# Optimization experiments

Measured on AMD Instinct MI355X. Metric: run time of the kernel, lower is better.

Reference implementation:

```python
import jax, jax.numpy as jnp
import numpy as np

B, N = 128, 196
ENC, DEC, ATT = 2048, 512, 512

def setup_inputs() -> dict:
    key = jax.random.key(0)
    ks = jax.random.split(key, 8)
    s_enc = 1.0 / np.sqrt(ENC)
    s_dec = 1.0 / np.sqrt(DEC)
    s_att = 1.0 / np.sqrt(ATT)
    return {
        "encoder_out": jax.random.normal(ks[0], (B, N, ENC), jnp.float32),
        "decoder_hidden": jax.random.normal(ks[1], (B, DEC), jnp.float32),
        "W_enc": jax.random.uniform(ks[2], (ENC, ATT), jnp.float32, -s_enc, s_enc),
        "b_enc": jax.random.uniform(ks[3], (ATT,), jnp.float32, -s_enc, s_enc),
        "W_dec": jax.random.uniform(ks[4], (DEC, ATT), jnp.float32, -s_dec, s_dec),
        "b_dec": jax.random.uniform(ks[5], (ATT,), jnp.float32, -s_dec, s_dec),
        "W_full": jax.random.uniform(ks[6], (ATT,), jnp.float32, -s_att, s_att),
        "b_full": jax.random.uniform(ks[7], (), jnp.float32, -s_att, s_att),
    }

def reference(encoder_out, decoder_hidden, W_enc, b_enc, W_dec, b_dec, W_full, b_full):
    # att1: [B, N, ATT]; att2: [B, 1, ATT]
    att1 = jnp.einsum('bne,ea->bna', encoder_out, W_enc) + b_enc
    att2 = decoder_hidden @ W_dec + b_dec
    combined = jax.nn.relu(att1 + att2[:, None, :])
    e = jnp.einsum('bna,a->bn', combined, W_full) + b_full  # [B, N]
    alpha = jax.nn.softmax(e, axis=1)
    attention_weighted_encoding = jnp.einsum('bne,bn->be', encoder_out, alpha)
    return attention_weighted_encoding, alpha
```

## Files before the change

kernel.cpp:

```cpp
#include <hip/hip_runtime.h>
#include <hip/hip_bf16.h>

#define BB   128
#define NN   196
#define MM   (BB*NN)
#define ENC  2048
#define ATT  512
#define DEC  512
#define BK   32
#define KSTEPS (ENC/BK)

using f32x4 = __attribute__((ext_vector_type(4))) float;
using s16x8 = __attribute__((ext_vector_type(8))) short;
using u16x4 = __attribute__((ext_vector_type(4))) unsigned short;
using u16x8 = __attribute__((ext_vector_type(8))) unsigned short;

__device__ __forceinline__ short f2bf(float f) {
    union { __hip_bfloat16 h; short s; } u;
    u.h = __float2bfloat16(f);
    return u.s;
}
__device__ __forceinline__ float bf2f(unsigned short u) {
    union { unsigned int i; float f; } v;
    v.i = ((unsigned int)u) << 16;
    return v.f;
}

__global__ void transpose_convert_kernel(const float* __restrict__ W,
                                         unsigned short* __restrict__ Wt) {
    __shared__ float tile[32][33];
    const int a0 = blockIdx.x * 32;
    const int k0 = blockIdx.y * 32;
    const int tx = threadIdx.x & 31, ty = threadIdx.x >> 5;
    #pragma unroll
    for (int i = 0; i < 32; i += 8)
        tile[ty + i][tx] = W[(size_t)(k0 + ty + i) * ATT + a0 + tx];
    __syncthreads();
    #pragma unroll
    for (int i = 0; i < 32; i += 8) {
        union { __hip_bfloat16 h; unsigned short u; } v;
        v.h = __float2bfloat16(tile[tx][ty + i]);
        Wt[(size_t)(a0 + ty + i) * ENC + k0 + tx] = v.u;
    }
}

__global__ __launch_bounds__(256)
void enc_cvt_kernel(const float* __restrict__ enc,
                    unsigned short* __restrict__ encb) {
    const size_t row = blockIdx.x;
    const int t = threadIdx.x;
    const float* in = enc + row * ENC + t * 8;
    f32x4 a = *(const f32x4*)in;
    f32x4 b = *(const f32x4*)(in + 4);
    u16x8 o;
    #pragma unroll
    for (int j = 0; j < 4; ++j) {
        o[j]     = (unsigned short)f2bf(a[j]);
        o[4 + j] = (unsigned short)f2bf(b[j]);
    }
    *(u16x8*)(encb + row * ENC + t * 8) = o;
}

__global__ void att2_kernel(const float* __restrict__ dec,
                            const float* __restrict__ Wd,
                            const float* __restrict__ bd,
                            const float* __restrict__ benc,
                            float* __restrict__ att2) {
    const int b  = blockIdx.x;
    const int c0 = blockIdx.y * 64;
    const int t  = threadIdx.x;
    const int cl = t & 63, kg = t >> 6;
    __shared__ float sdec[DEC];
    __shared__ float red[4][64];
    sdec[t]       = dec[b * DEC + t];
    sdec[t + 256] = dec[b * DEC + t + 256];
    __syncthreads();
    float acc = 0.f;
    const float* wp = Wd + c0 + cl;
    #pragma unroll 8
    for (int k = kg * 128; k < kg * 128 + 128; ++k)
        acc += sdec[k] * wp[(size_t)k * ATT];
    red[kg][cl] = acc;
    __syncthreads();
    if (t < 64) {
        float s = red[0][t] + red[1][t] + red[2][t] + red[3][t];
        att2[b * ATT + c0 + t] = s + bd[c0 + t] + benc[c0 + t];
    }
}

__global__ __launch_bounds__(256, 4)
void gemm_bf16_kernel(const unsigned short* __restrict__ encb,
                      const unsigned short* __restrict__ Wt,
                      const float* __restrict__ att2,
                      const float* __restrict__ Wf,
                      float* __restrict__ e_part) {
    __shared__ unsigned short sA[64 * 32];
    __shared__ unsigned short sB[256 * 32];
    __shared__ float e_sm[64];

    const int t    = threadIdx.x;
    const int lane = t & 63;
    const int w    = t >> 6;
    const int aBlk  = blockIdx.x;
    const int mBase = blockIdx.y * 64;
    const int aBase = aBlk * 256;
    const int r = lane & 15, q = lane >> 4;

    const unsigned short* gA = encb + (size_t)(mBase + (t >> 2)) * ENC + (t & 3) * 8;
    const unsigned short* gB[4];
    #pragma unroll
    for (int i = 0; i < 4; ++i) {
        int s = i * 256 + t;
        gB[i] = Wt + (size_t)(aBase + (s >> 2)) * ENC + (s & 3) * 8;
    }

    int offA[4];
    #pragma unroll
    for (int mi = 0; mi < 4; ++mi)
        offA[mi] = (mi * 16 + r) * 64 + q * 16;
    int offB[4];
    #pragma unroll
    for (int ni = 0; ni < 4; ++ni)
        offB[ni] = (w * 64 + ni * 16 + r) * 64 + q * 16;

    f32x4 acc[4][4] = {};

    #pragma unroll 1
    for (int ks = 0; ks < KSTEPS; ++ks) {
        __builtin_amdgcn_global_load_lds(
            (const __attribute__((address_space(1))) void*)(gA + (size_t)ks * BK),
            (__attribute__((address_space(3))) void*)((char*)sA + t * 16),
            16, 0, 0);
        #pragma unroll
        for (int i = 0; i < 4; ++i)
            __builtin_amdgcn_global_load_lds(
                (const __attribute__((address_space(1))) void*)(gB[i] + (size_t)ks * BK),
                (__attribute__((address_space(3))) void*)((char*)sB + (i * 256 + t) * 16),
                16, 0, 0);
        __syncthreads();

        s16x8 af[4], bf[4];
        #pragma unroll
        for (int mi = 0; mi < 4; ++mi)
            af[mi] = *(const s16x8*)((const char*)sA + offA[mi]);
        #pragma unroll
        for (int ni = 0; ni < 4; ++ni)
            bf[ni] = *(const s16x8*)((const char*)sB + offB[ni]);

        #pragma unroll
        for (int mi = 0; mi < 4; ++mi)
            #pragma unroll
            for (int ni = 0; ni < 4; ++ni)
                acc[mi][ni] = __builtin_amdgcn_mfma_f32_16x16x32_bf16(
                    af[mi], bf[ni], acc[mi][ni], 0, 0, 0);
        __syncthreads();
    }

    if (t < 64) e_sm[t] = 0.f;
    __syncthreads();

    float wfv[4];
    #pragma unroll
    for (int ni = 0; ni < 4; ++ni)
        wfv[ni] = Wf[aBase + w * 64 + ni * 16 + r];

    #pragma unroll
    for (int mi = 0; mi < 4; ++mi) {
        #pragma unroll
        for (int reg = 0; reg < 4; ++reg) {
            int lrow = mi * 16 + q * 4 + reg;
            int gm = mBase + lrow;
            int b = gm / NN;
            const float* a2 = att2 + b * ATT + aBase + w * 64;
            float rs = 0.f;
            #pragma unroll
            for (int ni = 0; ni < 4; ++ni) {
                float v = acc[mi][ni][reg] + a2[ni * 16 + r];
                rs += fmaxf(v, 0.f) * wfv[ni];
            }
            rs += __shfl_xor(rs, 1);
            rs += __shfl_xor(rs, 2);
            rs += __shfl_xor(rs, 4);
            rs += __shfl_xor(rs, 8);
            if (r == 0) atomicAdd(&e_sm[lrow], rs);
        }
    }
    __syncthreads();
    if (t < 64)
        e_part[(size_t)aBlk * MM + mBase + t] = e_sm[t];
}

__global__ __launch_bounds__(256, 5)
void gemm_e_kernel(const float* __restrict__ enc,
                   const unsigned short* __restrict__ Wt,
                   const float* __restrict__ att2,
                   const float* __restrict__ Wf,
                   float* __restrict__ e_part) {
    __shared__ float sA[64 * 32];
    __shared__ unsigned short sB[128 * 32];
    __shared__ float e_sm[64];

    const int t    = threadIdx.x;
    const int lane = t & 63;
    const int w    = t >> 6;
    const int aBlk  = blockIdx.x;
    const int mBase = blockIdx.y * 64;
    const int aBase = aBlk * 128;
    const int r = lane & 15, q = lane >> 4;

    const float* gA[2];
    #pragma unroll
    for (int i = 0; i < 2; ++i) {
        int s = i * 256 + t;
        int row = s >> 3, ck = s & 7;
        int g = ck ^ (row & 7);
        gA[i] = enc + (size_t)(mBase + row) * ENC + g * 4;
    }
    const unsigned short* gB[2];
    #pragma unroll
    for (int i = 0; i < 2; ++i) {
        int s = i * 256 + t;
        int row = s >> 2, ck = s & 3;
        int g = ck ^ ((row & 3) ^ ((row >> 2) & 3));
        gB[i] = Wt + (size_t)(aBase + row) * ENC + g * 8;
    }

    int offA[4][2];
    #pragma unroll
    for (int mi = 0; mi < 4; ++mi) {
        int row = mi * 16 + r;
        offA[mi][0] = row * 128 + ((2 * q)     ^ (row & 7)) * 16;
        offA[mi][1] = row * 128 + ((2 * q + 1) ^ (row & 7)) * 16;
    }
    int offB[2];
    #pragma unroll
    for (int ni = 0; ni < 2; ++ni) {
        int col = w * 32 + ni * 16 + r;
        offB[ni] = col * 64 + (q ^ ((col & 3) ^ ((col >> 2) & 3))) * 16;
    }

    f32x4 acc[4][2] = {};

    #pragma unroll 1
    for (int ks = 0; ks < KSTEPS; ++ks) {
        #pragma unroll
        for (int i = 0; i < 2; ++i)
            __builtin_amdgcn_global_load_lds(
                (const __attribute__((address_space(1))) void*)(gA[i] + (size_t)ks * BK),
                (__attribute__((address_space(3))) void*)((char*)sA + (i * 256 + w * 64) * 16),
                16, 0, 0);
        #pragma unroll
        for (int i = 0; i < 2; ++i)
            __builtin_amdgcn_global_load_lds(
                (const __attribute__((address_space(1))) void*)(gB[i] + (size_t)ks * BK),
                (__attribute__((address_space(3))) void*)((char*)sB + (i * 256 + w * 64) * 16),
                16, 0, 0);
        __syncthreads();

        s16x8 af[4], bf[2];
        #pragma unroll
        for (int mi = 0; mi < 4; ++mi) {
            f32x4 f0 = *(const f32x4*)((const char*)sA + offA[mi][0]);
            f32x4 f1 = *(const f32x4*)((const char*)sA + offA[mi][1]);
            s16x8 a;
            #pragma unroll
            for (int j = 0; j < 4; ++j) { a[j] = f2bf(f0[j]); a[4 + j] = f2bf(f1[j]); }
            af[mi] = a;
        }
        #pragma unroll
        for (int ni = 0; ni < 2; ++ni)
            bf[ni] = *(const s16x8*)((const char*)sB + offB[ni]);

        #pragma unroll
        for (int mi = 0; mi < 4; ++mi)
            #pragma unroll
            for (int ni = 0; ni < 2; ++ni)
                acc[mi][ni] = __builtin_amdgcn_mfma_f32_16x16x32_bf16(
                    af[mi], bf[ni], acc[mi][ni], 0, 0, 0);
        __syncthreads();
    }

    if (t < 64) e_sm[t] = 0.f;
    __syncthreads();

    float wfv[2];
    #pragma unroll
    for (int ni = 0; ni < 2; ++ni)
        wfv[ni] = Wf[aBase + w * 32 + ni * 16 + r];

    #pragma unroll
    for (int mi = 0; mi < 4; ++mi) {
        #pragma unroll
        for (int reg = 0; reg < 4; ++reg) {
            int lrow = mi * 16 + q * 4 + reg;
            int gm = mBase + lrow;
            int b = gm / NN;
            const float* a2 = att2 + b * ATT + aBase + w * 32;
            float rs = 0.f;
            #pragma unroll
            for (int ni = 0; ni < 2; ++ni) {
                float v = acc[mi][ni][reg] + a2[ni * 16 + r];
                rs += fmaxf(v, 0.f) * wfv[ni];
            }
            rs += __shfl_xor(rs, 1);
            rs += __shfl_xor(rs, 2);
            rs += __shfl_xor(rs, 4);
            rs += __shfl_xor(rs, 8);
            if (r == 0) atomicAdd(&e_sm[lrow], rs);
        }
    }
    __syncthreads();
    if (t < 64)
        e_part[(size_t)aBlk * MM + mBase + t] = e_sm[t];
}

__global__ void softmax_kernel(const float* __restrict__ e_part,
                               const float* __restrict__ b_full,
                               float* __restrict__ out,
                               float* __restrict__ alpha_ws,
                               int nparts) {
    const int b = blockIdx.x;
    const int t = threadIdx.x;
    __shared__ float sm[256];

    float v = -3.0e38f;
    if (t < NN) {
        int gm = b * NN + t;
        float s = b_full[0];
        for (int p = 0; p < nparts; ++p) s += e_part[(size_t)p * MM + gm];
        v = s;
    }
    sm[t] = v;
    __syncthreads();
    for (int s = 128; s > 0; s >>= 1) {
        if (t < s) sm[t] = fmaxf(sm[t], sm[t + s]);
        __syncthreads();
    }
    float mx = sm[0];
    __syncthreads();
    float ex = (t < NN) ? __expf(v - mx) : 0.f;
    sm[t] = ex;
    __syncthreads();
    for (int s = 128; s > 0; s >>= 1) {
        if (t < s) sm[t] += sm[t + s];
        __syncthreads();
    }
    float inv = 1.0f / sm[0];
    if (t < NN) {
        float a = ex * inv;
        out[BB * ENC + b * NN + t] = a;
        alpha_ws[b * NN + t] = a;
    }
}

__global__ __launch_bounds__(256)
void awe_bf16_kernel(const unsigned short* __restrict__ encb,
                     const float* __restrict__ alpha_ws,
                     float* __restrict__ out) {
    const int b = blockIdx.x, chunk = blockIdx.y;
    const int t = threadIdx.x;
    __shared__ float al[NN];
    if (t < NN) al[t] = alpha_ws[b * NN + t];
    __syncthreads();

    const unsigned short* ep = encb + (size_t)b * NN * ENC + chunk * 1024 + t * 4;
    f32x4 acc0 = {}, acc1 = {}, acc2 = {}, acc3 = {};
    #pragma unroll 2
    for (int n = 0; n < NN; n += 4) {
        u16x4 v0 = *(const u16x4*)(ep + (size_t)(n + 0) * ENC);
        u16x4 v1 = *(const u16x4*)(ep + (size_t)(n + 1) * ENC);
        u16x4 v2 = *(const u16x4*)(ep + (size_t)(n + 2) * ENC);
        u16x4 v3 = *(const u16x4*)(ep + (size_t)(n + 3) * ENC);
        #pragma unroll
        for (int j = 0; j < 4; ++j) {
            acc0[j] += bf2f(v0[j]) * al[n];
            acc1[j] += bf2f(v1[j]) * al[n + 1];
            acc2[j] += bf2f(v2[j]) * al[n + 2];
            acc3[j] += bf2f(v3[j]) * al[n + 3];
        }
    }
    f32x4 s = (acc0 + acc1) + (acc2 + acc3);
    *(f32x4*)(out + (size_t)b * ENC + chunk * 1024 + t * 4) = s;
}

__global__ __launch_bounds__(256)
void awe_kernel(const float* __restrict__ enc,
                const float* __restrict__ alpha_ws,
                float* __restrict__ out) {
    const int b = blockIdx.x, chunk = blockIdx.y;
    const int t = threadIdx.x;
    __shared__ float al[NN];
    if (t < NN) al[t] = alpha_ws[b * NN + t];
    __syncthreads();

    const float* ep = enc + (size_t)b * NN * ENC + chunk * 1024 + t * 4;
    f32x4 acc0 = {}, acc1 = {}, acc2 = {}, acc3 = {};
    #pragma unroll 2
    for (int n = 0; n < NN; n += 4) {
        f32x4 v0 = *(const f32x4*)(ep + (size_t)(n + 0) * ENC);
        f32x4 v1 = *(const f32x4*)(ep + (size_t)(n + 1) * ENC);
        f32x4 v2 = *(const f32x4*)(ep + (size_t)(n + 2) * ENC);
        f32x4 v3 = *(const f32x4*)(ep + (size_t)(n + 3) * ENC);
        acc0 += v0 * al[n];
        acc1 += v1 * al[n + 1];
        acc2 += v2 * al[n + 2];
        acc3 += v3 * al[n + 3];
    }
    f32x4 s = (acc0 + acc1) + (acc2 + acc3);
    *(f32x4*)(out + (size_t)b * ENC + chunk * 1024 + t * 4) = s;
}

extern "C" void kernel_launch(void* const* d_in, const int* in_sizes, int n_in,
                              void* d_out, int out_size, void* d_ws, size_t ws_size,
                              hipStream_t stream) {
    const float* enc    = (const float*)d_in[0];
    const float* dec    = (const float*)d_in[1];
    const float* W_enc  = (const float*)d_in[2];
    const float* b_enc  = (const float*)d_in[3];
    const float* W_dec  = (const float*)d_in[4];
    const float* b_dec  = (const float*)d_in[5];
    const float* W_full = (const float*)d_in[6];
    const float* b_full = (const float*)d_in[7];
    float* out = (float*)d_out;

    char* ws = (char*)d_ws;
    unsigned short* Wt = (unsigned short*)ws;
    float* att2     = (float*)(ws + 2097152);
    float* e_part   = (float*)(ws + 2359296);
    float* alpha_ws = (float*)(ws + 2760704);
    unsigned short* encb = (unsigned short*)(ws + 3145728);
    const size_t WS_NEED = 3145728 + (size_t)MM * ENC * 2;

    transpose_convert_kernel<<<dim3(ATT / 32, ENC / 32), 256, 0, stream>>>(W_enc, Wt);
    att2_kernel<<<dim3(BB, 8), 256, 0, stream>>>(dec, W_dec, b_dec, b_enc, att2);

    if (ws_size >= WS_NEED) {
        enc_cvt_kernel<<<MM, 256, 0, stream>>>(enc, encb);
        gemm_bf16_kernel<<<dim3(2, MM / 64), 256, 0, stream>>>(encb, Wt, att2, W_full, e_part);
        softmax_kernel<<<BB, 256, 0, stream>>>(e_part, b_full, out, alpha_ws, 2);
        awe_bf16_kernel<<<dim3(BB, 2), 256, 0, stream>>>(encb, alpha_ws, out);
    } else {
        gemm_e_kernel<<<dim3(4, MM / 64), 256, 0, stream>>>(enc, Wt, att2, W_full, e_part);
        softmax_kernel<<<BB, 256, 0, stream>>>(e_part, b_full, out, alpha_ws, 4);
        awe_kernel<<<dim3(BB, 2), 256, 0, stream>>>(enc, alpha_ws, out);
    }
}
```

Before: 445.1 us.

## Double-buffer LDS tiles in bf16 GEMM and remap layout for conflict-free fragment reads

The GEMM main loop now uses two LDS buffers, so global-to-LDS loads for the next K step are issued before the MFMAs on the current one, with one barrier per iteration instead of two. The global-load mapping is also reordered so each MFMA fragment sits contiguously in LDS (lane*16 offsets), which removes strided shared-memory reads and likely bank conflicts. The cost is double the LDS footprint, and launch bounds drop from 4 to 3 blocks per SM, so occupancy may fall.

Result: slower. 513.5 us (+15.4%).

```diff
diff --git a/kernel.cpp b/kernel.cpp
--- a/kernel.cpp
+++ b/kernel.cpp
@@ -88,14 +88,14 @@
     }
 }
 
-__global__ __launch_bounds__(256, 4)
+__global__ __launch_bounds__(256, 3)
 void gemm_bf16_kernel(const unsigned short* __restrict__ encb,
                       const unsigned short* __restrict__ Wt,
                       const float* __restrict__ att2,
                       const float* __restrict__ Wf,
                       float* __restrict__ e_part) {
-    __shared__ unsigned short sA[64 * 32];
-    __shared__ unsigned short sB[256 * 32];
+    __shared__ unsigned short sA[2][64 * 32];
+    __shared__ unsigned short sB[2][256 * 32];
     __shared__ float e_sm[64];
 
     const int t    = threadIdx.x;
@@ -106,58 +106,61 @@
     const int aBase = aBlk * 256;
     const int r = lane & 15, q = lane >> 4;
 
-    const unsigned short* gA = encb + (size_t)(mBase + (t >> 2)) * ENC + (t & 3) * 8;
+    if (t < 64) e_sm[t] = 0.f;
+
+    const unsigned short* gA =
+        encb + (size_t)(mBase + ((t >> 6) << 4) + (t & 15)) * ENC + ((t >> 4) & 3) * 8;
     const unsigned short* gB[4];
     #pragma unroll
     for (int i = 0; i < 4; ++i) {
         int s = i * 256 + t;
-        gB[i] = Wt + (size_t)(aBase + (s >> 2)) * ENC + (s & 3) * 8;
-    }
-
-    int offA[4];
-    #pragma unroll
-    for (int mi = 0; mi < 4; ++mi)
-        offA[mi] = (mi * 16 + r) * 64 + q * 16;
-    int offB[4];
-    #pragma unroll
-    for (int ni = 0; ni < 4; ++ni)
-        offB[ni] = (w * 64 + ni * 16 + r) * 64 + q * 16;
+        gB[i] = Wt + (size_t)(aBase + ((s >> 6) << 4) + (t & 15)) * ENC + ((t >> 4) & 3) * 8;
+    }
 
     f32x4 acc[4][4] = {};
 
-    #pragma unroll 1
-    for (int ks = 0; ks < KSTEPS; ++ks) {
+    auto stage = [&](int buf, int ks) {
         __builtin_amdgcn_global_load_lds(
             (const __attribute__((address_space(1))) void*)(gA + (size_t)ks * BK),
-            (__attribute__((address_space(3))) void*)((char*)sA + t * 16),
+            (__attribute__((address_space(3))) void*)((char*)sA[buf] + t * 16),
             16, 0, 0);
         #pragma unroll
         for (int i = 0; i < 4; ++i)
             __builtin_amdgcn_global_load_lds(
                 (const __attribute__((address_space(1))) void*)(gB[i] + (size_t)ks * BK),
-                (__attribute__((address_space(3))) void*)((char*)sB + (i * 256 + t) * 16),
+                (__attribute__((address_space(3))) void*)((char*)sB[buf] + (i * 256 + t) * 16),
                 16, 0, 0);
-        __syncthreads();
-
+    };
+
+    auto compute = [&](int buf) {
+        const char* pA = (const char*)sA[buf];
+        const char* pB = (const char*)sB[buf];
         s16x8 af[4], bf[4];
         #pragma unroll
         for (int mi = 0; mi < 4; ++mi)
-            af[mi] = *(const s16x8*)((const char*)sA + offA[mi]);
+            af[mi] = *(const s16x8*)(pA + mi * 1024 + lane * 16);
         #pragma unroll
         for (int ni = 0; ni < 4; ++ni)
-            bf[ni] = *(const s16x8*)((const char*)sB + offB[ni]);
-
+            bf[ni] = *(const s16x8*)(pB + (w * 4 + ni) * 1024 + lane * 16);
         #pragma unroll
         for (int mi = 0; mi < 4; ++mi)
             #pragma unroll
             for (int ni = 0; ni < 4; ++ni)
                 acc[mi][ni] = __builtin_amdgcn_mfma_f32_16x16x32_bf16(
                     af[mi], bf[ni], acc[mi][ni], 0, 0, 0);
+    };
+
+    stage(0, 0);
+    __syncthreads();
+    int cur = 0;
+    #pragma unroll 1
+    for (int ks = 0; ks < KSTEPS - 1; ++ks) {
+        stage(cur ^ 1, ks + 1);
+        compute(cur);
         __syncthreads();
-    }
-
-    if (t < 64) e_sm[t] = 0.f;
-    __syncthreads();
+        cur ^= 1;
+    }
+    compute(cur);
 
     float wfv[4];
     #pragma unroll
```

## Retile bf16 GEMM to 64x128 tiles with BK=64 and fragment-ordered LDS layout

Applied to the files above, without the earlier changes.

The bf16 attention-score GEMM now uses 64x128 output tiles instead of 64x256, launching four column blocks per row tile, and doubles the K step to 64 so each barrier pair covers two MFMA sub-steps. Global-to-LDS loads are remapped so each lane's MFMA fragment sits contiguously in shared memory, which is meant to avoid bank conflicts on the fragment reads. Per-wave accumulators shrink from 4x4 to 4x2, which frees registers and doubles grid size to improve occupancy. In exchange, encoder rows are re-read by twice as many blocks, and softmax must sum four partial score buffers.

New measurement: 502.9 us. 1.13x slower.

```diff
diff --git a/kernel.cpp b/kernel.cpp
--- a/kernel.cpp
+++ b/kernel.cpp
@@ -9,6 +9,8 @@
 #define DEC  512
 #define BK   32
 #define KSTEPS (ENC/BK)
+#define BK2  64
+#define KSTEPS2 (ENC/BK2)
 
 using f32x4 = __attribute__((ext_vector_type(4))) float;
 using s16x8 = __attribute__((ext_vector_type(8))) short;
@@ -94,8 +96,8 @@
                       const float* __restrict__ att2,
                       const float* __restrict__ Wf,
                       float* __restrict__ e_part) {
-    __shared__ unsigned short sA[64 * 32];
-    __shared__ unsigned short sB[256 * 32];
+    __shared__ unsigned short sA[512 * 8];
+    __shared__ unsigned short sB[1024 * 8];
     __shared__ float e_sm[64];
 
     const int t    = threadIdx.x;
@@ -103,66 +105,69 @@
     const int w    = t >> 6;
     const int aBlk  = blockIdx.x;
     const int mBase = blockIdx.y * 64;
-    const int aBase = aBlk * 256;
+    const int aBase = aBlk * 128;
     const int r = lane & 15, q = lane >> 4;
 
-    const unsigned short* gA = encb + (size_t)(mBase + (t >> 2)) * ENC + (t & 3) * 8;
+    if (t < 64) e_sm[t] = 0.f;
+
+    const unsigned short* gA[2];
+    #pragma unroll
+    for (int i = 0; i < 2; ++i) {
+        int s = i * 256 + t;
+        int row = (((s >> 6) & 3) << 4) + (s & 15);
+        int col = ((s >> 8) << 5) + (((s >> 4) & 3) << 3);
+        gA[i] = encb + (size_t)(mBase + row) * ENC + col;
+    }
     const unsigned short* gB[4];
     #pragma unroll
     for (int i = 0; i < 4; ++i) {
         int s = i * 256 + t;
-        gB[i] = Wt + (size_t)(aBase + (s >> 2)) * ENC + (s & 3) * 8;
-    }
-
-    int offA[4];
-    #pragma unroll
-    for (int mi = 0; mi < 4; ++mi)
-        offA[mi] = (mi * 16 + r) * 64 + q * 16;
-    int offB[4];
-    #pragma unroll
-    for (int ni = 0; ni < 4; ++ni)
-        offB[ni] = (w * 64 + ni * 16 + r) * 64 + q * 16;
-
-    f32x4 acc[4][4] = {};
+        int row = (((s >> 6) & 7) << 4) + (s & 15);
+        int col = ((s >> 9) << 5) + (((s >> 4) & 3) << 3);
+        gB[i] = Wt + (size_t)(aBase + row) * ENC + col;
+    }
+
+    f32x4 acc[4][2] = {};
 
     #pragma unroll 1
-    for (int ks = 0; ks < KSTEPS; ++ks) {
-        __builtin_amdgcn_global_load_lds(
-            (const __attribute__((address_space(1))) void*)(gA + (size_t)ks * BK),
-            (__attribute__((address_space(3))) void*)((char*)sA + t * 16),
-            16, 0, 0);
+    for (int ks = 0; ks < KSTEPS2; ++ks) {
+        #pragma unroll
+        for (int i = 0; i < 2; ++i)
+            __builtin_amdgcn_global_load_lds(
+                (const __attribute__((address_space(1))) void*)(gA[i] + (size_t)ks * BK2),
+                (__attribute__((address_space(3))) void*)((char*)sA + (i * 256 + t) * 16),
+                16, 0, 0);
         #pragma unroll
         for (int i = 0; i < 4; ++i)
             __builtin_amdgcn_global_load_lds(
-                (const __attribute__((address_space(1))) void*)(gB[i] + (size_t)ks * BK),
+                (const __attribute__((address_space(1))) void*)(gB[i] + (size_t)ks * BK2),
                 (__attribute__((address_space(3))) void*)((char*)sB + (i * 256 + t) * 16),
                 16, 0, 0);
         __syncthreads();
 
-        s16x8 af[4], bf[4];
-        #pragma unroll
-        for (int mi = 0; mi < 4; ++mi)
-            af[mi] = *(const s16x8*)((const char*)sA + offA[mi]);
-        #pragma unroll
-        for (int ni = 0; ni < 4; ++ni)
-            bf[ni] = *(const s16x8*)((const char*)sB + offB[ni]);
-
-        #pragma unroll
-        for (int mi = 0; mi < 4; ++mi)
-            #pragma unroll
-            for (int ni = 0; ni < 4; ++ni)
-                acc[mi][ni] = __builtin_amdgcn_mfma_f32_16x16x32_bf16(
-                    af[mi], bf[ni], acc[mi][ni], 0, 0, 0);
-        __syncthreads();
-    }
-
-    if (t < 64) e_sm[t] = 0.f;
-    __syncthreads();
-
-    float wfv[4];
-    #pragma unroll
-    for (int ni = 0; ni < 4; ++ni)
-        wfv[ni] = Wf[aBase + w * 64 + ni * 16 + r];
+        #pragma unroll
+        for (int kk = 0; kk < 2; ++kk) {
+            s16x8 af[4], bf[2];
+            #pragma unroll
+            for (int mi = 0; mi < 4; ++mi)
+                af[mi] = *(const s16x8*)((const char*)sA + ((kk * 4 + mi) * 64 + lane) * 16);
+            #pragma unroll
+            for (int ni = 0; ni < 2; ++ni)
+                bf[ni] = *(const s16x8*)((const char*)sB + ((kk * 8 + w * 2 + ni) * 64 + lane) * 16);
+            #pragma unroll
+            for (int mi = 0; mi < 4; ++mi)
+                #pragma unroll
+                for (int ni = 0; ni < 2; ++ni)
+                    acc[mi][ni] = __builtin_amdgcn_mfma_f32_16x16x32_bf16(
+                        af[mi], bf[ni], acc[mi][ni], 0, 0, 0);
+        }
+        __syncthreads();
+    }
+
+    float wfv[2];
+    #pragma unroll
+    for (int ni = 0; ni < 2; ++ni)
+        wfv[ni] = Wf[aBase + w * 32 + ni * 16 + r];
 
     #pragma unroll
     for (int mi = 0; mi < 4; ++mi) {
@@ -171,10 +176,10 @@
             int lrow = mi * 16 + q * 4 + reg;
             int gm = mBase + lrow;
             int b = gm / NN;
-            const float* a2 = att2 + b * ATT + aBase + w * 64;
+            const float* a2 = att2 + b * ATT + aBase + w * 32;
             float rs = 0.f;
             #pragma unroll
-            for (int ni = 0; ni < 4; ++ni) {
+            for (int ni = 0; ni < 2; ++ni) {
                 float v = acc[mi][ni][reg] + a2[ni * 16 + r];
                 rs += fmaxf(v, 0.f) * wfv[ni];
             }
@@ -436,8 +441,8 @@
 
     if (ws_size >= WS_NEED) {
         enc_cvt_kernel<<<MM, 256, 0, stream>>>(enc, encb);
-        gemm_bf16_kernel<<<dim3(2, MM / 64), 256, 0, stream>>>(encb, Wt, att2, W_full, e_part);
-        softmax_kernel<<<BB, 256, 0, stream>>>(e_part, b_full, out, alpha_ws, 2);
+        gemm_bf16_kernel<<<dim3(4, MM / 64), 256, 0, stream>>>(encb, Wt, att2, W_full, e_part);
+        softmax_kernel<<<BB, 256, 0, stream>>>(e_part, b_full, out, alpha_ws, 4);
         awe_bf16_kernel<<<dim3(BB, 2), 256, 0, stream>>>(encb, alpha_ws, out);
     } else {
         gemm_e_kernel<<<dim3(4, MM / 64), 256, 0, stream>>>(enc, Wt, att2, W_full, e_part);
```

## Enlarge bf16 GEMM tile to 128x256 with 8 waves and fragment-ordered LDS

Applied to the files above, without the earlier changes.

The bf16 GEMM block grows from 64 rows to 128 rows with 512 threads (8 waves arranged 2x4), so each block of W_enc loaded into LDS is reused across twice as many encoder rows. Global-to-LDS loads are remapped so that each wave reads its MFMA fragments contiguously by lane, replacing the padded row-major LDS offsets. The aim is to cut redundant global traffic for W and bank conflicts on LDS reads. The cost is fewer blocks in the grid and larger blocks that may lower occupancy.

New measurement: 440.4 us. About the same (-1.1%).

```diff
diff --git a/kernel.cpp b/kernel.cpp
--- a/kernel.cpp
+++ b/kernel.cpp
@@ -9,6 +9,8 @@
 #define DEC  512
 #define BK   32
 #define KSTEPS (ENC/BK)
+#define BM   128
+#define BA   256
 
 using f32x4 = __attribute__((ext_vector_type(4))) float;
 using s16x8 = __attribute__((ext_vector_type(8))) short;
@@ -88,40 +90,36 @@
     }
 }
 
-__global__ __launch_bounds__(256, 4)
+__global__ __launch_bounds__(512, 4)
 void gemm_bf16_kernel(const unsigned short* __restrict__ encb,
                       const unsigned short* __restrict__ Wt,
                       const float* __restrict__ att2,
                       const float* __restrict__ Wf,
                       float* __restrict__ e_part) {
-    __shared__ unsigned short sA[64 * 32];
-    __shared__ unsigned short sB[256 * 32];
-    __shared__ float e_sm[64];
+    __shared__ unsigned short sA[512 * 8];
+    __shared__ unsigned short sB[1024 * 8];
+    __shared__ float e_sm[BM];
 
     const int t    = threadIdx.x;
     const int lane = t & 63;
     const int w    = t >> 6;
+    const int wm   = w >> 2;
+    const int wa   = w & 3;
     const int aBlk  = blockIdx.x;
-    const int mBase = blockIdx.y * 64;
-    const int aBase = aBlk * 256;
+    const int mBase = blockIdx.y * BM;
+    const int aBase = aBlk * BA;
     const int r = lane & 15, q = lane >> 4;
 
-    const unsigned short* gA = encb + (size_t)(mBase + (t >> 2)) * ENC + (t & 3) * 8;
-    const unsigned short* gB[4];
-    #pragma unroll
-    for (int i = 0; i < 4; ++i) {
-        int s = i * 256 + t;
-        gB[i] = Wt + (size_t)(aBase + (s >> 2)) * ENC + (s & 3) * 8;
-    }
-
-    int offA[4];
-    #pragma unroll
-    for (int mi = 0; mi < 4; ++mi)
-        offA[mi] = (mi * 16 + r) * 64 + q * 16;
-    int offB[4];
-    #pragma unroll
-    for (int ni = 0; ni < 4; ++ni)
-        offB[ni] = (w * 64 + ni * 16 + r) * 64 + q * 16;
+    if (t < BM) e_sm[t] = 0.f;
+
+    const unsigned short* gA =
+        encb + (size_t)(mBase + ((t >> 6) << 4) + (t & 15)) * ENC + ((t >> 4) & 3) * 8;
+    const unsigned short* gB[2];
+    #pragma unroll
+    for (int i = 0; i < 2; ++i) {
+        int s = i * 512 + t;
+        gB[i] = Wt + (size_t)(aBase + ((s >> 6) << 4) + (s & 15)) * ENC + ((s >> 4) & 3) * 8;
+    }
 
     f32x4 acc[4][4] = {};
 
@@ -132,21 +130,20 @@
             (__attribute__((address_space(3))) void*)((char*)sA + t * 16),
             16, 0, 0);
         #pragma unroll
-        for (int i = 0; i < 4; ++i)
+        for (int i = 0; i < 2; ++i)
             __builtin_amdgcn_global_load_lds(
                 (const __attribute__((address_space(1))) void*)(gB[i] + (size_t)ks * BK),
-                (__attribute__((address_space(3))) void*)((char*)sB + (i * 256 + t) * 16),
+                (__attribute__((address_space(3))) void*)((char*)sB + (i * 512 + t) * 16),
                 16, 0, 0);
         __syncthreads();
 
         s16x8 af[4], bf[4];
         #pragma unroll
         for (int mi = 0; mi < 4; ++mi)
-            af[mi] = *(const s16x8*)((const char*)sA + offA[mi]);
+            af[mi] = *(const s16x8*)((const char*)sA + (((wm * 4 + mi) * 64 + lane) * 16));
         #pragma unroll
         for (int ni = 0; ni < 4; ++ni)
-            bf[ni] = *(const s16x8*)((const char*)sB + offB[ni]);
-
+            bf[ni] = *(const s16x8*)((const char*)sB + (((wa * 4 + ni) * 64 + lane) * 16));
         #pragma unroll
         for (int mi = 0; mi < 4; ++mi)
             #pragma unroll
@@ -156,22 +153,19 @@
         __syncthreads();
     }
 
-    if (t < 64) e_sm[t] = 0.f;
-    __syncthreads();
-
     float wfv[4];
     #pragma unroll
     for (int ni = 0; ni < 4; ++ni)
-        wfv[ni] = Wf[aBase + w * 64 + ni * 16 + r];
+        wfv[ni] = Wf[aBase + wa * 64 + ni * 16 + r];
 
     #pragma unroll
     for (int mi = 0; mi < 4; ++mi) {
         #pragma unroll
         for (int reg = 0; reg < 4; ++reg) {
-            int lrow = mi * 16 + q * 4 + reg;
+            int lrow = wm * 64 + mi * 16 + q * 4 + reg;
             int gm = mBase + lrow;
             int b = gm / NN;
-            const float* a2 = att2 + b * ATT + aBase + w * 64;
+            const float* a2 = att2 + b * ATT + aBase + wa * 64;
             float rs = 0.f;
             #pragma unroll
             for (int ni = 0; ni < 4; ++ni) {
@@ -186,7 +180,7 @@
         }
     }
     __syncthreads();
-    if (t < 64)
+    if (t < BM)
         e_part[(size_t)aBlk * MM + mBase + t] = e_sm[t];
 }
 
@@ -436,7 +430,7 @@
 
     if (ws_size >= WS_NEED) {
         enc_cvt_kernel<<<MM, 256, 0, stream>>>(enc, encb);
-        gemm_bf16_kernel<<<dim3(2, MM / 64), 256, 0, stream>>>(encb, Wt, att2, W_full, e_part);
+        gemm_bf16_kernel<<<dim3(ATT / BA, MM / BM), 512, 0, stream>>>(encb, Wt, att2, W_full, e_part);
         softmax_kernel<<<BB, 256, 0, stream>>>(e_part, b_full, out, alpha_ws, 2);
         awe_bf16_kernel<<<dim3(BB, 2), 256, 0, stream>>>(encb, alpha_ws, out);
     } else {
```
